# Kernel tuning notes

Hardware: AMD Instinct MI355X
Metric: run time of the kernel (lower is better)

The kernel has to match this reference:

```python
import jax, jax.numpy as jnp
import numpy as np

SHAPES = [(64, 64), (32, 32), (16, 16), (8, 8)]  # (H, W) per level, sum HW = 5440
DIMS, NH, NLVL, NPTS, D_HEIGHT, NCAM, NQ, BS = 256, 8, 4, 8, 4, 6, 10000, 1


def ms_deform_attn(value, shapes, loc, attw):
    # value [B, sumHW, nH, dh]; loc [B, nq, nH, L, P, 2] in [0,1]; attw [B, nq, nH, L, P]
    B, _, nH, dh = value.shape
    nq, P = loc.shape[1], loc.shape[4]
    out = jnp.zeros((B, nH, nq, dh), value.dtype)
    start = 0
    for lvl, (h, w) in enumerate(shapes):
        v = value[:, start:start + h * w].transpose(0, 2, 1, 3)  # [B,nH,hw,dh]
        start += h * w
        l = loc[:, :, :, lvl].transpose(0, 2, 1, 3, 4)  # [B,nH,nq,P,2]
        x = l[..., 0] * w - 0.5
        y = l[..., 1] * h - 0.5
        x0, y0 = jnp.floor(x), jnp.floor(y)
        acc = jnp.zeros((B, nH, nq, P, dh), value.dtype)
        for dy in (0.0, 1.0):
            for dx in (0.0, 1.0):
                cx, cy = x0 + dx, y0 + dy
                wgt = (1.0 - jnp.abs(x - cx)) * (1.0 - jnp.abs(y - cy))
                valid = (cx >= 0) & (cx < w) & (cy >= 0) & (cy < h)
                xi = jnp.clip(cx, 0, w - 1).astype(jnp.int32)
                yi = jnp.clip(cy, 0, h - 1).astype(jnp.int32)
                idx = (yi * w + xi).reshape(B, nH, -1)  # [B,nH,nq*P]
                g = jnp.take_along_axis(v, idx[..., None], axis=2).reshape(B, nH, nq, P, dh)
                acc = acc + jnp.where(valid, wgt, 0.0)[..., None] * g
        aw = attw[:, :, :, lvl].transpose(0, 2, 1, 3)  # [B,nH,nq,P]
        out = out + jnp.einsum('bhqp,bhqpd->bhqd', aw, acc)
    return out.transpose(0, 2, 1, 3).reshape(B, nq, nH * dh)


def setup_inputs() -> dict:
    key = jax.random.key(0)
    ks = jax.random.split(key, 16)
    l = sum(h * w for h, w in SHAPES)
    s = 1.0 / np.sqrt(DIMS)
    inp = {
        'query': jax.random.normal(ks[0], (BS, NQ, DIMS), jnp.float32),
        'key': jax.random.normal(ks[1], (NCAM, l, BS, DIMS), jnp.float32),
        'value': jax.random.normal(ks[2], (NCAM, l, BS, DIMS), jnp.float32),
        'ref_points': jax.random.uniform(ks[3], (NCAM, BS, NQ, D_HEIGHT, 2), jnp.float32),
        'vox_mask': jax.random.randint(ks[4], (NCAM, BS, NQ, D_HEIGHT), 0, 2) > 0,
        'spatial_shapes': np.array(SHAPES, dtype=np.int64),
        'level_start_index': np.array([0, 4096, 5120, 5376], dtype=np.int64),
        'value_W': jax.random.uniform(ks[5], (DIMS, DIMS), jnp.float32, -s, s),
        'value_b': jnp.zeros((DIMS,), jnp.float32),
        'off_W': jax.random.normal(ks[6], (DIMS, NH * NLVL * NPTS * 2), jnp.float32) * 0.01,
        'off_b': jax.random.normal(ks[7], (NH * NLVL * NPTS * 2,), jnp.float32) * 0.1,
        'attw_W': jax.random.normal(ks[8], (DIMS, NH * NLVL * NPTS), jnp.float32) * 0.02,
        'attw_b': jnp.zeros((NH * NLVL * NPTS,), jnp.float32),
        'out_W': jax.random.uniform(ks[9], (DIMS, DIMS), jnp.float32, -s, s),
        'out_b': jnp.zeros((DIMS,), jnp.float32),
    }
    return inp


def reference(query, key, value, ref_points, vox_mask, spatial_shapes, level_start_index,
              value_W, value_b, off_W, off_b, attw_W, attw_b, out_W, out_b):
    shapes = [(int(h), int(w)) for h, w in np.asarray(spatial_shapes)]
    bs, nq, dims = query.shape
    cam = vox_mask.shape[0]
    B = bs * cam
    nH = NH
    dh = dims // nH
    Lv, P, D = len(shapes), NPTS, ref_points.shape[3]

    # value_proj; key unused by deformable attention math
    v = value.transpose(2, 0, 1, 3).reshape(B, -1, dims)
    v = (v @ value_W + value_b).reshape(B, -1, nH, dh)

    # rebatch: every camera sees the full (batch-0 visible) query set; padded
    # entries in the original are discarded, so computing all and masking is exact.
    q = jnp.broadcast_to(query[:, None], (bs, cam, nq, dims)).reshape(B, nq, dims)

    off = (q @ off_W + off_b).reshape(B, nq, nH, Lv, P, 2)
    attw = jax.nn.softmax((q @ attw_W + attw_b).reshape(B, nq, nH, Lv * P), -1)
    attw = attw.reshape(B, nq, nH, Lv, P)

    norm = jnp.array([[w, h] for h, w in shapes], q.dtype)  # [Lv,2] -> (W,H)
    off = off / norm[None, None, None, :, None, :]

    ref_rb = ref_points.transpose(1, 0, 2, 3, 4).reshape(B, nq, D, 2)
    off = off.reshape(B, nq, nH, Lv, P // D, D, 2)
    loc = (ref_rb[:, :, None, None, None] + off).reshape(B, nq, nH, Lv, P, 2)

    out = ms_deform_attn(v, shapes, loc, attw).reshape(bs, cam, nq, dims)

    valid = (vox_mask[:, 0].sum(-1) > 0).astype(q.dtype)  # [cam,nq] (batch-0 indexes, as original)
    slots = jnp.einsum('cq,bcqd->bqd', valid, out)
    count = (vox_mask.sum(-1) > 0).transpose(1, 2, 0).sum(-1).astype(q.dtype)
    count = jnp.maximum(count, 1.0)
    slots = slots / count[..., None]
    slots = slots @ out_W + out_b
    return slots + query  # dropout = identity (eval); inp_residual = query
```

## Files before the change

kernel.cpp:

```cpp
#include <hip/hip_runtime.h>


typedef unsigned short ushort_t;
typedef unsigned int uint_t;
typedef __attribute__((ext_vector_type(8))) short bf16x8;
typedef __attribute__((ext_vector_type(4))) float f32x4;
typedef __attribute__((ext_vector_type(2))) float f32x2;

__device__ __forceinline__ float bf2f(ushort_t u) {
    return __uint_as_float(((uint_t)u) << 16);
}
__device__ __forceinline__ ushort_t f2bf(float f) {
    uint_t i = __float_as_uint(f);
    uint_t r = i + 0x7fffu + ((i >> 16) & 1u);
    return (ushort_t)(r >> 16);
}

__global__ __launch_bounds__(256) void prep_k(
    const float* __restrict__ value, const float* __restrict__ query,
    const float* __restrict__ Wv, const float* __restrict__ Wo,
    const float* __restrict__ Wf, const float* __restrict__ Wa,
    ushort_t* __restrict__ value_bf, ushort_t* __restrict__ query_bf,
    ushort_t* __restrict__ Tv, ushort_t* __restrict__ To,
    ushort_t* __restrict__ Tqk) {
    __shared__ float tile[32][33];
    const int b = blockIdx.x;
    const int tid = threadIdx.x;

    if (b < 5330) {
        const float* src;
        ushort_t* dst;
        int i, n8;
        if (b < 4080) { src = value; dst = value_bf; i = b * 256 + tid;           n8 = 1044480; }
        else          { src = query; dst = query_bf; i = (b - 4080) * 256 + tid;  n8 = 320000; }
        if (i >= n8) return;
        const float4 v0 = *(const float4*)(src + (size_t)i * 8);
        const float4 v1 = *(const float4*)(src + (size_t)i * 8 + 4);
        const bf16x8 pk = {
            (short)f2bf(v0.x), (short)f2bf(v0.y), (short)f2bf(v0.z), (short)f2bf(v0.w),
            (short)f2bf(v1.x), (short)f2bf(v1.y), (short)f2bf(v1.z), (short)f2bf(v1.w)};
        *(bf16x8*)(dst + (size_t)i * 8) = pk;
        return;
    }

    const int b2 = b - 5330;
    const int z   = b2 >> 7;
    const int rem = b2 & 127;
    const int k0 = (rem & 7) * 32;
    const int n0 = (rem >> 3) * 32;
    const float* W;
    ushort_t* T;
    int N;
    if (z == 0)      { W = Wv; T = Tv;              N = 256; }
    else if (z == 1) { W = Wo; T = To;              N = 256; }
    else if (z == 2) { W = Wf; T = Tqk;             N = 512; }
    else             { W = Wa; T = Tqk + 512 * 256; N = 256; }
    if (n0 >= N) return;

    const int tx = tid & 31;
    const int ty = tid >> 5;
    #pragma unroll
    for (int r = 0; r < 4; ++r) {
        const int k = ty + r * 8;
        tile[k][tx] = W[(size_t)(k0 + k) * N + n0 + tx];
    }
    __syncthreads();
    #pragma unroll
    for (int r = 0; r < 4; ++r) {
        const int n = ty + r * 8;
        T[(size_t)(n0 + n) * 256 + k0 + tx] = f2bf(tile[tx][n]);
    }
}

template <bool OUT_BF16, bool RESID>
__global__ __launch_bounds__(256) void gemm_mfma(
    const ushort_t* __restrict__ A, const ushort_t* __restrict__ Wt,
    const float* __restrict__ bias0, const float* __restrict__ bias1, int split,
    const float* __restrict__ resid, void* __restrict__ Cv, int M, int N) {
    __shared__ ushort_t sA[2][128][32];
    __shared__ ushort_t sB[2][128][32];

    const int m0 = blockIdx.x * 128;
    const int n0 = blockIdx.y * 128;
    const int t    = threadIdx.x;
    const int lane = t & 63;
    const int w    = t >> 6;
    const int wr   = w >> 1, wc = w & 1;

    const int srow = t >> 2;
    const int skof = (t & 3) * 8;

    const bool am0 = (m0 + srow) < M;
    const bool am1 = (m0 + 64 + srow) < M;
    const ushort_t* Ap0 = A + (size_t)(m0 + srow) * 256 + skof;
    const ushort_t* Ap1 = Ap0 + (size_t)64 * 256;
    const ushort_t* Bp0 = Wt + (size_t)(n0 + srow) * 256 + skof;
    const ushort_t* Bp1 = Bp0 + (size_t)64 * 256;

    f32x4 acc[4][4];
    #pragma unroll
    for (int i = 0; i < 4; ++i)
        #pragma unroll
        for (int j = 0; j < 4; ++j)
            acc[i][j] = (f32x4){0.f, 0.f, 0.f, 0.f};

    const bf16x8 zz = {0, 0, 0, 0, 0, 0, 0, 0};

    {
        const bf16x8 a0 = am0 ? *(const bf16x8*)(Ap0) : zz;
        const bf16x8 a1 = am1 ? *(const bf16x8*)(Ap1) : zz;
        const bf16x8 b0 = *(const bf16x8*)(Bp0);
        const bf16x8 b1 = *(const bf16x8*)(Bp1);
        *(bf16x8*)(&sA[0][srow][skof])      = a0;
        *(bf16x8*)(&sA[0][64 + srow][skof]) = a1;
        *(bf16x8*)(&sB[0][srow][skof])      = b0;
        *(bf16x8*)(&sB[0][64 + srow][skof]) = b1;
    }
    __syncthreads();

    const int rl = lane & 15;
    const int kq = (lane >> 4) * 8;

    for (int k = 0; k < 8; ++k) {
        const int buf = k & 1;

        bf16x8 na0 = zz, na1 = zz, nb0 = zz, nb1 = zz;
        if (k < 7) {
            const int ko = (k + 1) * 32;
            if (am0) na0 = *(const bf16x8*)(Ap0 + ko);
            if (am1) na1 = *(const bf16x8*)(Ap1 + ko);
            nb0 = *(const bf16x8*)(Bp0 + ko);
            nb1 = *(const bf16x8*)(Bp1 + ko);
        }

        bf16x8 af[4], bfr[4];
        #pragma unroll
        for (int i = 0; i < 4; ++i)
            af[i] = *(const bf16x8*)(&sA[buf][wr * 64 + i * 16 + rl][kq]);
        #pragma unroll
        for (int j = 0; j < 4; ++j)
            bfr[j] = *(const bf16x8*)(&sB[buf][wc * 64 + j * 16 + rl][kq]);
        #pragma unroll
        for (int i = 0; i < 4; ++i)
            #pragma unroll
            for (int j = 0; j < 4; ++j)
                acc[i][j] = __builtin_amdgcn_mfma_f32_16x16x32_bf16(
                    af[i], bfr[j], acc[i][j], 0, 0, 0);

        if (k < 7) {
            __syncthreads();
            *(bf16x8*)(&sA[buf ^ 1][srow][skof])      = na0;
            *(bf16x8*)(&sA[buf ^ 1][64 + srow][skof]) = na1;
            *(bf16x8*)(&sB[buf ^ 1][srow][skof])      = nb0;
            *(bf16x8*)(&sB[buf ^ 1][64 + srow][skof]) = nb1;
            __syncthreads();
        }
    }

    const int col_l = lane & 15;
    const int rq    = (lane >> 4) * 4;
    #pragma unroll
    for (int j = 0; j < 4; ++j) {
        const int gn = n0 + wc * 64 + j * 16 + col_l;
        const float bj = (gn < split) ? bias0[gn] : bias1[gn - split];
        #pragma unroll
        for (int i = 0; i < 4; ++i) {
            #pragma unroll
            for (int r = 0; r < 4; ++r) {
                const int gm = m0 + wr * 64 + i * 16 + rq + r;
                if (gm >= M) continue;
                float v = acc[i][j][r] + bj;
                if (RESID) v += resid[(size_t)gm * N + gn];
                if (OUT_BF16)
                    ((ushort_t*)Cv)[(size_t)gm * N + gn] = f2bf(v);
                else
                    ((float*)Cv)[(size_t)gm * N + gn] = v;
            }
        }
    }
}

__global__ __launch_bounds__(256) void sample_k(
    const float* __restrict__ qkcat,
    const float* __restrict__ refp,
    const int* __restrict__ vox,
    const ushort_t* __restrict__ vproj,
    ushort_t* __restrict__ slots) {
    const int q   = blockIdx.x;
    const int tid = threadIdx.x;
    const int h     = tid >> 5;
    const int lp    = tid & 31;
    const int slice = (tid >> 2) & 7;
    const int g     = tid & 3;

    __shared__ float s_valid[8];
    __shared__ int   s_ci[4][256];
    __shared__ float s_cw[4][256];
    __shared__ float s_red[256][8];

    if (tid < 6) {
        const int base = (tid * 10000 + q) * 4;
        const int mm = vox[base] | vox[base + 1] | vox[base + 2] | vox[base + 3];
        s_valid[tid] = mm ? 1.0f : 0.0f;
    }

    const float a = qkcat[(size_t)q * 768 + 512 + tid];
    float mx = a;
    #pragma unroll
    for (int o = 16; o >= 1; o >>= 1) mx = fmaxf(mx, __shfl_xor(mx, o));
    const float e = __expf(a - mx);
    float se = e;
    #pragma unroll
    for (int o = 16; o >= 1; o >>= 1) se += __shfl_xor(se, o);
    const float aw = e / se;

    const int lvl = lp >> 3;
    const int p   = lp & 7;
    const int dd  = p & 3;
    const int   Sarr[4]   = {64, 32, 16, 8};
    const int   Lstart[4] = {0, 4096, 5120, 5376};
    const int   S  = Sarr[lvl];
    const float Sf = (float)S;
    const int   lstart = Lstart[lvl];
    const float ox = qkcat[(size_t)q * 768 + h * 64 + lvl * 16 + p * 2 + 0] / Sf;
    const float oy = qkcat[(size_t)q * 768 + h * 64 + lvl * 16 + p * 2 + 1] / Sf;

    __syncthreads();
    const float cnt = s_valid[0] + s_valid[1] + s_valid[2] +
                      s_valid[3] + s_valid[4] + s_valid[5];

    f32x2 acc2[4] = {{0.f, 0.f}, {0.f, 0.f}, {0.f, 0.f}, {0.f, 0.f}};
    const ushort_t* vp = vproj + (g << 3);

    for (int c = 0; c < 6; ++c) {
        if (s_valid[c] == 0.0f) continue;

        {
            const int rbase = ((c * 10000 + q) * 4 + dd) * 2;
            const float rx = refp[rbase + 0];
            const float ry = refp[rbase + 1];
            const float x  = (rx + ox) * Sf - 0.5f;
            const float y  = (ry + oy) * Sf - 0.5f;
            const float x0 = floorf(x), y0 = floorf(y);
            #pragma unroll
            for (int k = 0; k < 4; ++k) {
                const float cx = x0 + (float)(k & 1);
                const float cy = y0 + (float)(k >> 1);
                const float wgt = (1.0f - fabsf(x - cx)) * (1.0f - fabsf(y - cy));
                const bool ok = (cx >= 0.0f) & (cx < Sf) & (cy >= 0.0f) & (cy < Sf);
                const int xi = (int)fminf(fmaxf(cx, 0.0f), Sf - 1.0f);
                const int yi = (int)fminf(fmaxf(cy, 0.0f), Sf - 1.0f);
                s_ci[k][tid] = (c * 5440 + lstart + yi * S + xi) * 256 + h * 32;
                s_cw[k][tid] = ok ? wgt * aw : 0.0f;
            }
        }
        __syncthreads();

        #pragma unroll
        for (int j = 0; j < 4; ++j) {
            const int el = h * 32 + slice * 4 + j;
            const int i0 = s_ci[0][el], i1 = s_ci[1][el];
            const int i2 = s_ci[2][el], i3 = s_ci[3][el];
            const float w0 = s_cw[0][el], w1 = s_cw[1][el];
            const float w2 = s_cw[2][el], w3 = s_cw[3][el];
            const uint4 v0 = *(const uint4*)(vp + i0);
            const uint4 v1 = *(const uint4*)(vp + i1);
            const uint4 v2 = *(const uint4*)(vp + i2);
            const uint4 v3 = *(const uint4*)(vp + i3);
            const f32x2 W0 = {w0, w0}, W1 = {w1, w1}, W2 = {w2, w2}, W3 = {w3, w3};
            acc2[0] += W0 * (f32x2){__uint_as_float(v0.x << 16),
                                    __uint_as_float(v0.x & 0xffff0000u)};
            acc2[1] += W0 * (f32x2){__uint_as_float(v0.y << 16),
                                    __uint_as_float(v0.y & 0xffff0000u)};
            acc2[2] += W0 * (f32x2){__uint_as_float(v0.z << 16),
                                    __uint_as_float(v0.z & 0xffff0000u)};
            acc2[3] += W0 * (f32x2){__uint_as_float(v0.w << 16),
                                    __uint_as_float(v0.w & 0xffff0000u)};
            acc2[0] += W1 * (f32x2){__uint_as_float(v1.x << 16),
                                    __uint_as_float(v1.x & 0xffff0000u)};
            acc2[1] += W1 * (f32x2){__uint_as_float(v1.y << 16),
                                    __uint_as_float(v1.y & 0xffff0000u)};
            acc2[2] += W1 * (f32x2){__uint_as_float(v1.z << 16),
                                    __uint_as_float(v1.z & 0xffff0000u)};
            acc2[3] += W1 * (f32x2){__uint_as_float(v1.w << 16),
                                    __uint_as_float(v1.w & 0xffff0000u)};
            acc2[0] += W2 * (f32x2){__uint_as_float(v2.x << 16),
                                    __uint_as_float(v2.x & 0xffff0000u)};
            acc2[1] += W2 * (f32x2){__uint_as_float(v2.y << 16),
                                    __uint_as_float(v2.y & 0xffff0000u)};
            acc2[2] += W2 * (f32x2){__uint_as_float(v2.z << 16),
                                    __uint_as_float(v2.z & 0xffff0000u)};
            acc2[3] += W2 * (f32x2){__uint_as_float(v2.w << 16),
                                    __uint_as_float(v2.w & 0xffff0000u)};
            acc2[0] += W3 * (f32x2){__uint_as_float(v3.x << 16),
                                    __uint_as_float(v3.x & 0xffff0000u)};
            acc2[1] += W3 * (f32x2){__uint_as_float(v3.y << 16),
                                    __uint_as_float(v3.y & 0xffff0000u)};
            acc2[2] += W3 * (f32x2){__uint_as_float(v3.z << 16),
                                    __uint_as_float(v3.z & 0xffff0000u)};
            acc2[3] += W3 * (f32x2){__uint_as_float(v3.w << 16),
                                    __uint_as_float(v3.w & 0xffff0000u)};
        }
        __syncthreads();
    }

    #pragma unroll
    for (int n = 0; n < 4; ++n) {
        s_red[tid][2 * n]     = acc2[n].x;
        s_red[tid][2 * n + 1] = acc2[n].y;
    }
    __syncthreads();

    const int cch = tid & 31;
    float sum = 0.0f;
    #pragma unroll
    for (int s = 0; s < 8; ++s)
        sum += s_red[h * 32 + s * 4 + (cch >> 3)][cch & 7];

    slots[(size_t)q * 256 + tid] = f2bf(sum / fmaxf(cnt, 1.0f));
}

extern "C" void kernel_launch(void* const* d_in, const int* in_sizes, int n_in,
                              void* d_out, int out_size, void* d_ws, size_t ws_size,
                              hipStream_t stream) {
    const float* query   = (const float*)d_in[0];
    const float* value   = (const float*)d_in[2];
    const float* refp    = (const float*)d_in[3];
    const int*   vox     = (const int*)d_in[4];
    const float* value_W = (const float*)d_in[7];
    const float* value_b = (const float*)d_in[8];
    const float* off_W   = (const float*)d_in[9];
    const float* off_b   = (const float*)d_in[10];
    const float* attw_W  = (const float*)d_in[11];
    const float* attw_b  = (const float*)d_in[12];
    const float* out_W   = (const float*)d_in[13];
    const float* out_b   = (const float*)d_in[14];
    float* out = (float*)d_out;

    char* ws = (char*)d_ws;
    ushort_t* vproj    = (ushort_t*)ws;
    ushort_t* value_bf = (ushort_t*)(ws + 16711680);
    float*    qkcat    = (float*)   (ws + 16711680);
    ushort_t* query_bf = (ushort_t*)(ws + 47431680);
    ushort_t* slots    = (ushort_t*)(ws + 47431680);
    ushort_t* value_Wt = (ushort_t*)(ws + 52551680);
    ushort_t* out_Wt   = (ushort_t*)(ws + 52551680 + 131072);
    ushort_t* qk_Wt    = (ushort_t*)(ws + 52551680 + 262144);

    prep_k<<<5842, 256, 0, stream>>>(value, query, value_W, out_W, off_W, attw_W,
                                     value_bf, query_bf, value_Wt, out_Wt, qk_Wt);
    gemm_mfma<true, false><<<dim3(255, 2), 256, 0, stream>>>(
        value_bf, value_Wt, value_b, value_b, 256, nullptr,
        (void*)vproj, 32640, 256);
    gemm_mfma<false, false><<<dim3(79, 6), 256, 0, stream>>>(
        query_bf, qk_Wt, off_b, attw_b, 512, nullptr,
        (void*)qkcat, 10000, 768);
    sample_k<<<10000, 256, 0, stream>>>(qkcat, refp, vox, vproj, slots);
    gemm_mfma<false, true><<<dim3(79, 2), 256, 0, stream>>>(
        slots, out_Wt, out_b, out_b, 256, query, (void*)out, 10000, 256);
}
```

Measured before the change: 337.8 us.

## Fuse all stages into one persistent cooperative kernel with grid syncs

Replaces the five separate launches (prep, two projection GEMMs, sampling, output GEMM) with a single persistent cooperative kernel. Blocks loop over work units and are separated by grid-wide barriers, with a shared-memory union reused across stages. It also shrinks the GEMM tiles to 64x64 and stores the offset/attention projection in bf16 instead of fp32, halving that buffer's traffic. The intent is to remove launch gaps and tail effects. In exchange it adds grid-sync cost, gives smaller GEMM tiles less reuse, caps the grid at 1024 blocks, and lowers the precision of the sampling offsets and attention logits.

```diff
diff --git a/kernel.cpp b/kernel.cpp
--- a/kernel.cpp
+++ b/kernel.cpp
@@ -1,4 +1,5 @@
 #include <hip/hip_runtime.h>
+#include <hip/hip_cooperative_groups.h>
 
 
 typedef unsigned short ushort_t;
@@ -16,23 +17,31 @@
     return (ushort_t)(r >> 16);
 }
 
-__global__ __launch_bounds__(256) void prep_k(
+struct GemmSmem  { ushort_t sA[2][64][32]; ushort_t sB[2][64][32]; };
+struct SampleSmem {
+    float valid[8];
+    int   ci[4][256];
+    float cw[4][256];
+    float red[256][8];
+};
+struct PrepSmem  { float tile[32][33]; };
+union SmemAll { GemmSmem g; SampleSmem s; PrepSmem p; };
+
+__device__ __forceinline__ void prep_unit(
+    int u, PrepSmem* sp,
     const float* __restrict__ value, const float* __restrict__ query,
     const float* __restrict__ Wv, const float* __restrict__ Wo,
     const float* __restrict__ Wf, const float* __restrict__ Wa,
     ushort_t* __restrict__ value_bf, ushort_t* __restrict__ query_bf,
     ushort_t* __restrict__ Tv, ushort_t* __restrict__ To,
     ushort_t* __restrict__ Tqk) {
-    __shared__ float tile[32][33];
-    const int b = blockIdx.x;
     const int tid = threadIdx.x;
-
-    if (b < 5330) {
+    if (u < 5330) {
         const float* src;
         ushort_t* dst;
         int i, n8;
-        if (b < 4080) { src = value; dst = value_bf; i = b * 256 + tid;           n8 = 1044480; }
-        else          { src = query; dst = query_bf; i = (b - 4080) * 256 + tid;  n8 = 320000; }
+        if (u < 4080) { src = value; dst = value_bf; i = u * 256 + tid;          n8 = 1044480; }
+        else          { src = query; dst = query_bf; i = (u - 4080) * 256 + tid; n8 = 320000; }
         if (i >= n8) return;
         const float4 v0 = *(const float4*)(src + (size_t)i * 8);
         const float4 v1 = *(const float4*)(src + (size_t)i * 8 + 4);
@@ -42,8 +51,7 @@
         *(bf16x8*)(dst + (size_t)i * 8) = pk;
         return;
     }
-
-    const int b2 = b - 5330;
+    const int b2 = u - 5330;
     const int z   = b2 >> 7;
     const int rem = b2 & 127;
     const int k0 = (rem & 7) * 32;
@@ -62,149 +70,109 @@
     #pragma unroll
     for (int r = 0; r < 4; ++r) {
         const int k = ty + r * 8;
-        tile[k][tx] = W[(size_t)(k0 + k) * N + n0 + tx];
+        sp->tile[k][tx] = W[(size_t)(k0 + k) * N + n0 + tx];
     }
     __syncthreads();
     #pragma unroll
     for (int r = 0; r < 4; ++r) {
         const int n = ty + r * 8;
-        T[(size_t)(n0 + n) * 256 + k0 + tx] = f2bf(tile[tx][n]);
-    }
+        T[(size_t)(n0 + n) * 256 + k0 + tx] = f2bf(sp->tile[tx][n]);
+    }
+    __syncthreads();
 }
 
 template <bool OUT_BF16, bool RESID>
-__global__ __launch_bounds__(256) void gemm_mfma(
+__device__ __forceinline__ void gemm64_tile(
+    GemmSmem* sm,
     const ushort_t* __restrict__ A, const ushort_t* __restrict__ Wt,
     const float* __restrict__ bias0, const float* __restrict__ bias1, int split,
-    const float* __restrict__ resid, void* __restrict__ Cv, int M, int N) {
-    __shared__ ushort_t sA[2][128][32];
-    __shared__ ushort_t sB[2][128][32];
-
-    const int m0 = blockIdx.x * 128;
-    const int n0 = blockIdx.y * 128;
-    const int t    = threadIdx.x;
-    const int lane = t & 63;
-    const int w    = t >> 6;
-    const int wr   = w >> 1, wc = w & 1;
-
+    const float* __restrict__ resid, void* __restrict__ Cv,
+    int M, int N, int u) {
+    const int tn = N >> 6;
+    const int bx = u / tn;
+    const int by = u - bx * tn;
+    const int m0 = bx << 6, n0 = by << 6;
+    const int t = threadIdx.x, lane = t & 63, w = t >> 6;
     const int srow = t >> 2;
-    const int skof = (t & 3) * 8;
-
-    const bool am0 = (m0 + srow) < M;
-    const bool am1 = (m0 + 64 + srow) < M;
-    const ushort_t* Ap0 = A + (size_t)(m0 + srow) * 256 + skof;
-    const ushort_t* Ap1 = Ap0 + (size_t)64 * 256;
-    const ushort_t* Bp0 = Wt + (size_t)(n0 + srow) * 256 + skof;
-    const ushort_t* Bp1 = Bp0 + (size_t)64 * 256;
-
-    f32x4 acc[4][4];
-    #pragma unroll
-    for (int i = 0; i < 4; ++i)
+    const int skof = (t & 3) << 3;
+    const bool am = (m0 + srow) < M;
+    const ushort_t* Ap = A + (size_t)(m0 + srow) * 256 + skof;
+    const ushort_t* Bp = Wt + (size_t)(n0 + srow) * 256 + skof;
+    const bf16x8 zz = {0, 0, 0, 0, 0, 0, 0, 0};
+
+    f32x4 acc[4];
+    #pragma unroll
+    for (int j = 0; j < 4; ++j) acc[j] = (f32x4){0.f, 0.f, 0.f, 0.f};
+
+    *(bf16x8*)(&sm->sA[0][srow][skof]) = am ? *(const bf16x8*)Ap : zz;
+    *(bf16x8*)(&sm->sB[0][srow][skof]) = *(const bf16x8*)Bp;
+    __syncthreads();
+
+    const int rl = lane & 15;
+    const int kq = (lane >> 4) << 3;
+
+    for (int k = 0; k < 8; ++k) {
+        const int buf = k & 1;
+        bf16x8 na = zz, nb = zz;
+        if (k < 7) {
+            const int ko = (k + 1) << 5;
+            if (am) na = *(const bf16x8*)(Ap + ko);
+            nb = *(const bf16x8*)(Bp + ko);
+        }
+        const bf16x8 af = *(const bf16x8*)(&sm->sA[buf][(w << 4) + rl][kq]);
+        bf16x8 bfr[4];
         #pragma unroll
         for (int j = 0; j < 4; ++j)
-            acc[i][j] = (f32x4){0.f, 0.f, 0.f, 0.f};
-
-    const bf16x8 zz = {0, 0, 0, 0, 0, 0, 0, 0};
-
-    {
-        const bf16x8 a0 = am0 ? *(const bf16x8*)(Ap0) : zz;
-        const bf16x8 a1 = am1 ? *(const bf16x8*)(Ap1) : zz;
-        const bf16x8 b0 = *(const bf16x8*)(Bp0);
-        const bf16x8 b1 = *(const bf16x8*)(Bp1);
-        *(bf16x8*)(&sA[0][srow][skof])      = a0;
-        *(bf16x8*)(&sA[0][64 + srow][skof]) = a1;
-        *(bf16x8*)(&sB[0][srow][skof])      = b0;
-        *(bf16x8*)(&sB[0][64 + srow][skof]) = b1;
-    }
-    __syncthreads();
-
-    const int rl = lane & 15;
-    const int kq = (lane >> 4) * 8;
-
-    for (int k = 0; k < 8; ++k) {
-        const int buf = k & 1;
-
-        bf16x8 na0 = zz, na1 = zz, nb0 = zz, nb1 = zz;
-        if (k < 7) {
-            const int ko = (k + 1) * 32;
-            if (am0) na0 = *(const bf16x8*)(Ap0 + ko);
-            if (am1) na1 = *(const bf16x8*)(Ap1 + ko);
-            nb0 = *(const bf16x8*)(Bp0 + ko);
-            nb1 = *(const bf16x8*)(Bp1 + ko);
-        }
-
-        bf16x8 af[4], bfr[4];
-        #pragma unroll
-        for (int i = 0; i < 4; ++i)
-            af[i] = *(const bf16x8*)(&sA[buf][wr * 64 + i * 16 + rl][kq]);
+            bfr[j] = *(const bf16x8*)(&sm->sB[buf][(j << 4) + rl][kq]);
         #pragma unroll
         for (int j = 0; j < 4; ++j)
-            bfr[j] = *(const bf16x8*)(&sB[buf][wc * 64 + j * 16 + rl][kq]);
-        #pragma unroll
-        for (int i = 0; i < 4; ++i)
-            #pragma unroll
-            for (int j = 0; j < 4; ++j)
-                acc[i][j] = __builtin_amdgcn_mfma_f32_16x16x32_bf16(
-                    af[i], bfr[j], acc[i][j], 0, 0, 0);
-
+            acc[j] = __builtin_amdgcn_mfma_f32_16x16x32_bf16(af, bfr[j], acc[j], 0, 0, 0);
         if (k < 7) {
             __syncthreads();
-            *(bf16x8*)(&sA[buf ^ 1][srow][skof])      = na0;
-            *(bf16x8*)(&sA[buf ^ 1][64 + srow][skof]) = na1;
-            *(bf16x8*)(&sB[buf ^ 1][srow][skof])      = nb0;
-            *(bf16x8*)(&sB[buf ^ 1][64 + srow][skof]) = nb1;
+            *(bf16x8*)(&sm->sA[buf ^ 1][srow][skof]) = na;
+            *(bf16x8*)(&sm->sB[buf ^ 1][srow][skof]) = nb;
             __syncthreads();
         }
     }
 
     const int col_l = lane & 15;
-    const int rq    = (lane >> 4) * 4;
+    const int rq = (lane >> 4) << 2;
     #pragma unroll
     for (int j = 0; j < 4; ++j) {
-        const int gn = n0 + wc * 64 + j * 16 + col_l;
+        const int gn = n0 + (j << 4) + col_l;
         const float bj = (gn < split) ? bias0[gn] : bias1[gn - split];
         #pragma unroll
-        for (int i = 0; i < 4; ++i) {
-            #pragma unroll
-            for (int r = 0; r < 4; ++r) {
-                const int gm = m0 + wr * 64 + i * 16 + rq + r;
-                if (gm >= M) continue;
-                float v = acc[i][j][r] + bj;
-                if (RESID) v += resid[(size_t)gm * N + gn];
-                if (OUT_BF16)
-                    ((ushort_t*)Cv)[(size_t)gm * N + gn] = f2bf(v);
-                else
-                    ((float*)Cv)[(size_t)gm * N + gn] = v;
-            }
-        }
-    }
-}
-
-__global__ __launch_bounds__(256) void sample_k(
-    const float* __restrict__ qkcat,
-    const float* __restrict__ refp,
-    const int* __restrict__ vox,
-    const ushort_t* __restrict__ vproj,
+        for (int r = 0; r < 4; ++r) {
+            const int gm = m0 + (w << 4) + rq + r;
+            if (gm >= M) continue;
+            float v = acc[j][r] + bj;
+            if (RESID) v += resid[(size_t)gm * N + gn];
+            if (OUT_BF16)
+                ((ushort_t*)Cv)[(size_t)gm * N + gn] = f2bf(v);
+            else
+                ((float*)Cv)[(size_t)gm * N + gn] = v;
+        }
+    }
+}
+
+__device__ __forceinline__ void sample_unit(
+    int q, SampleSmem* ss,
+    const ushort_t* __restrict__ qkcat, const float* __restrict__ refp,
+    const int* __restrict__ vox, const ushort_t* __restrict__ vproj,
     ushort_t* __restrict__ slots) {
-    const int q   = blockIdx.x;
     const int tid = threadIdx.x;
     const int h     = tid >> 5;
     const int lp    = tid & 31;
     const int slice = (tid >> 2) & 7;
     const int g     = tid & 3;
 
-    __shared__ float s_valid[8];
-    __shared__ int   s_ci[4][256];
-    __shared__ float s_cw[4][256];
-    __shared__ float s_red[256][8];
-
     if (tid < 6) {
         const int base = (tid * 10000 + q) * 4;
         const int mm = vox[base] | vox[base + 1] | vox[base + 2] | vox[base + 3];
-        s_valid[tid] = mm ? 1.0f : 0.0f;
-    }
-
-    const float a = qkcat[(size_t)q * 768 + 512 + tid];
+        ss->valid[tid] = mm ? 1.0f : 0.0f;
+    }
+
+    const float a = bf2f(qkcat[(size_t)q * 768 + 512 + tid]);
     float mx = a;
     #pragma unroll
     for (int o = 16; o >= 1; o >>= 1) mx = fmaxf(mx, __shfl_xor(mx, o));
@@ -221,19 +189,20 @@
     const int   Lstart[4] = {0, 4096, 5120, 5376};
     const int   S  = Sarr[lvl];
     const float Sf = (float)S;
+    const float invSf = 1.0f / Sf;
     const int   lstart = Lstart[lvl];
-    const float ox = qkcat[(size_t)q * 768 + h * 64 + lvl * 16 + p * 2 + 0] / Sf;
-    const float oy = qkcat[(size_t)q * 768 + h * 64 + lvl * 16 + p * 2 + 1] / Sf;
-
-    __syncthreads();
-    const float cnt = s_valid[0] + s_valid[1] + s_valid[2] +
-                      s_valid[3] + s_valid[4] + s_valid[5];
+    const float ox = bf2f(qkcat[(size_t)q * 768 + h * 64 + lvl * 16 + p * 2 + 0]) * invSf;
+    const float oy = bf2f(qkcat[(size_t)q * 768 + h * 64 + lvl * 16 + p * 2 + 1]) * invSf;
+
+    __syncthreads();
+    const float cnt = ss->valid[0] + ss->valid[1] + ss->valid[2] +
+                      ss->valid[3] + ss->valid[4] + ss->valid[5];
 
     f32x2 acc2[4] = {{0.f, 0.f}, {0.f, 0.f}, {0.f, 0.f}, {0.f, 0.f}};
     const ushort_t* vp = vproj + (g << 3);
 
     for (int c = 0; c < 6; ++c) {
-        if (s_valid[c] == 0.0f) continue;
+        if (ss->valid[c] == 0.0f) continue;
 
         {
             const int rbase = ((c * 10000 + q) * 4 + dd) * 2;
@@ -250,8 +219,8 @@
                 const bool ok = (cx >= 0.0f) & (cx < Sf) & (cy >= 0.0f) & (cy < Sf);
                 const int xi = (int)fminf(fmaxf(cx, 0.0f), Sf - 1.0f);
                 const int yi = (int)fminf(fmaxf(cy, 0.0f), Sf - 1.0f);
-                s_ci[k][tid] = (c * 5440 + lstart + yi * S + xi) * 256 + h * 32;
-                s_cw[k][tid] = ok ? wgt * aw : 0.0f;
+                ss->ci[k][tid] = (c * 5440 + lstart + yi * S + xi) * 256 + h * 32;
+                ss->cw[k][tid] = ok ? wgt * aw : 0.0f;
             }
         }
         __syncthreads();
@@ -259,55 +228,39 @@
         #pragma unroll
         for (int j = 0; j < 4; ++j) {
             const int el = h * 32 + slice * 4 + j;
-            const int i0 = s_ci[0][el], i1 = s_ci[1][el];
-            const int i2 = s_ci[2][el], i3 = s_ci[3][el];
-            const float w0 = s_cw[0][el], w1 = s_cw[1][el];
-            const float w2 = s_cw[2][el], w3 = s_cw[3][el];
+            const int i0 = ss->ci[0][el], i1 = ss->ci[1][el];
+            const int i2 = ss->ci[2][el], i3 = ss->ci[3][el];
+            const float w0 = ss->cw[0][el], w1 = ss->cw[1][el];
+            const float w2 = ss->cw[2][el], w3 = ss->cw[3][el];
             const uint4 v0 = *(const uint4*)(vp + i0);
             const uint4 v1 = *(const uint4*)(vp + i1);
             const uint4 v2 = *(const uint4*)(vp + i2);
             const uint4 v3 = *(const uint4*)(vp + i3);
             const f32x2 W0 = {w0, w0}, W1 = {w1, w1}, W2 = {w2, w2}, W3 = {w3, w3};
-            acc2[0] += W0 * (f32x2){__uint_as_float(v0.x << 16),
-                                    __uint_as_float(v0.x & 0xffff0000u)};
-            acc2[1] += W0 * (f32x2){__uint_as_float(v0.y << 16),
-                                    __uint_as_float(v0.y & 0xffff0000u)};
-            acc2[2] += W0 * (f32x2){__uint_as_float(v0.z << 16),
-                                    __uint_as_float(v0.z & 0xffff0000u)};
-            acc2[3] += W0 * (f32x2){__uint_as_float(v0.w << 16),
-                                    __uint_as_float(v0.w & 0xffff0000u)};
-            acc2[0] += W1 * (f32x2){__uint_as_float(v1.x << 16),
-                                    __uint_as_float(v1.x & 0xffff0000u)};
-            acc2[1] += W1 * (f32x2){__uint_as_float(v1.y << 16),
-                                    __uint_as_float(v1.y & 0xffff0000u)};
-            acc2[2] += W1 * (f32x2){__uint_as_float(v1.z << 16),
-                                    __uint_as_float(v1.z & 0xffff0000u)};
-            acc2[3] += W1 * (f32x2){__uint_as_float(v1.w << 16),
-                                    __uint_as_float(v1.w & 0xffff0000u)};
-            acc2[0] += W2 * (f32x2){__uint_as_float(v2.x << 16),
-                                    __uint_as_float(v2.x & 0xffff0000u)};
-            acc2[1] += W2 * (f32x2){__uint_as_float(v2.y << 16),
-                                    __uint_as_float(v2.y & 0xffff0000u)};
-            acc2[2] += W2 * (f32x2){__uint_as_float(v2.z << 16),
-                                    __uint_as_float(v2.z & 0xffff0000u)};
-            acc2[3] += W2 * (f32x2){__uint_as_float(v2.w << 16),
-                                    __uint_as_float(v2.w & 0xffff0000u)};
-            acc2[0] += W3 * (f32x2){__uint_as_float(v3.x << 16),
-                                    __uint_as_float(v3.x & 0xffff0000u)};
-            acc2[1] += W3 * (f32x2){__uint_as_float(v3.y << 16),
-                                    __uint_as_float(v3.y & 0xffff0000u)};
-            acc2[2] += W3 * (f32x2){__uint_as_float(v3.z << 16),
-                                    __uint_as_float(v3.z & 0xffff0000u)};
-            acc2[3] += W3 * (f32x2){__uint_as_float(v3.w << 16),
-                                    __uint_as_float(v3.w & 0xffff0000u)};
+            acc2[0] += W0 * (f32x2){__uint_as_float(v0.x << 16), __uint_as_float(v0.x & 0xffff0000u)};
+            acc2[1] += W0 * (f32x2){__uint_as_float(v0.y << 16), __uint_as_float(v0.y & 0xffff0000u)};
+            acc2[2] += W0 * (f32x2){__uint_as_float(v0.z << 16), __uint_as_float(v0.z & 0xffff0000u)};
+            acc2[3] += W0 * (f32x2){__uint_as_float(v0.w << 16), __uint_as_float(v0.w & 0xffff0000u)};
+            acc2[0] += W1 * (f32x2){__uint_as_float(v1.x << 16), __uint_as_float(v1.x & 0xffff0000u)};
+            acc2[1] += W1 * (f32x2){__uint_as_float(v1.y << 16), __uint_as_float(v1.y & 0xffff0000u)};
+            acc2[2] += W1 * (f32x2){__uint_as_float(v1.z << 16), __uint_as_float(v1.z & 0xffff0000u)};
+            acc2[3] += W1 * (f32x2){__uint_as_float(v1.w << 16), __uint_as_float(v1.w & 0xffff0000u)};
+            acc2[0] += W2 * (f32x2){__uint_as_float(v2.x << 16), __uint_as_float(v2.x & 0xffff0000u)};
+            acc2[1] += W2 * (f32x2){__uint_as_float(v2.y << 16), __uint_as_float(v2.y & 0xffff0000u)};
+            acc2[2] += W2 * (f32x2){__uint_as_float(v2.z << 16), __uint_as_float(v2.z & 0xffff0000u)};
+            acc2[3] += W2 * (f32x2){__uint_as_float(v2.w << 16), __uint_as_float(v2.w & 0xffff0000u)};
+            acc2[0] += W3 * (f32x2){__uint_as_float(v3.x << 16), __uint_as_float(v3.x & 0xffff0000u)};
+            acc2[1] += W3 * (f32x2){__uint_as_float(v3.y << 16), __uint_as_float(v3.y & 0xffff0000u)};
+            acc2[2] += W3 * (f32x2){__uint_as_float(v3.z << 16), __uint_as_float(v3.z & 0xffff0000u)};
+            acc2[3] += W3 * (f32x2){__uint_as_float(v3.w << 16), __uint_as_float(v3.w & 0xffff0000u)};
         }
         __syncthreads();
     }
 
     #pragma unroll
     for (int n = 0; n < 4; ++n) {
-        s_red[tid][2 * n]     = acc2[n].x;
-        s_red[tid][2 * n + 1] = acc2[n].y;
+        ss->red[tid][2 * n]     = acc2[n].x;
+        ss->red[tid][2 * n + 1] = acc2[n].y;
     }
     __syncthreads();
 
@@ -315,9 +268,50 @@
     float sum = 0.0f;
     #pragma unroll
     for (int s = 0; s < 8; ++s)
-        sum += s_red[h * 32 + s * 4 + (cch >> 3)][cch & 7];
+        sum += ss->red[h * 32 + s * 4 + (cch >> 3)][cch & 7];
 
     slots[(size_t)q * 256 + tid] = f2bf(sum / fmaxf(cnt, 1.0f));
+}
+
+__global__ __launch_bounds__(256, 4) void fused_k(
+    const float* __restrict__ query, const float* __restrict__ value,
+    const float* __restrict__ refp, const int* __restrict__ vox,
+    const float* __restrict__ value_W, const float* __restrict__ value_b,
+    const float* __restrict__ off_W, const float* __restrict__ off_b,
+    const float* __restrict__ attw_W, const float* __restrict__ attw_b,
+    const float* __restrict__ out_W, const float* __restrict__ out_b,
+    float* __restrict__ out,
+    ushort_t* __restrict__ value_bf, ushort_t* __restrict__ query_bf,
+    ushort_t* __restrict__ vproj, ushort_t* __restrict__ qkcat,
+    ushort_t* __restrict__ slots,
+    ushort_t* __restrict__ value_Wt, ushort_t* __restrict__ out_Wt,
+    ushort_t* __restrict__ qk_Wt) {
+    cooperative_groups::grid_group grid = cooperative_groups::this_grid();
+    __shared__ SmemAll sm;
+    const int nb = gridDim.x;
+
+    for (int u = blockIdx.x; u < 5842; u += nb)
+        prep_unit(u, &sm.p, value, query, value_W, out_W, off_W, attw_W,
+                  value_bf, query_bf, value_Wt, out_Wt, qk_Wt);
+    grid.sync();
+
+    for (int u = blockIdx.x; u < 3924; u += nb) {
+        if (u < 2040)
+            gemm64_tile<true, false>(&sm.g, value_bf, value_Wt, value_b, value_b,
+                                     256, nullptr, (void*)vproj, 32640, 256, u);
+        else
+            gemm64_tile<true, false>(&sm.g, query_bf, qk_Wt, off_b, attw_b,
+                                     512, nullptr, (void*)qkcat, 10000, 768, u - 2040);
+    }
+    grid.sync();
+
+    for (int q = blockIdx.x; q < 10000; q += nb)
+        sample_unit(q, &sm.s, qkcat, refp, vox, vproj, slots);
+    grid.sync();
+
+    for (int u = blockIdx.x; u < 628; u += nb)
+        gemm64_tile<false, true>(&sm.g, slots, out_Wt, out_b, out_b, 256,
+                                 query, (void*)out, 10000, 256, u);
 }
 
 extern "C" void kernel_launch(void* const* d_in, const int* in_sizes, int n_in,
@@ -338,24 +332,28 @@
     float* out = (float*)d_out;
 
     char* ws = (char*)d_ws;
-    ushort_t* vproj    = (ushort_t*)ws;
+    ushort_t* vproj    = (ushort_t*)(ws);
     ushort_t* value_bf = (ushort_t*)(ws + 16711680);
-    float*    qkcat    = (float*)   (ws + 16711680);
-    ushort_t* query_bf = (ushort_t*)(ws + 47431680);
-    ushort_t* slots    = (ushort_t*)(ws + 47431680);
-    ushort_t* value_Wt = (ushort_t*)(ws + 52551680);
-    ushort_t* out_Wt   = (ushort_t*)(ws + 52551680 + 131072);
-    ushort_t* qk_Wt    = (ushort_t*)(ws + 52551680 + 262144);
-
-    prep_k<<<5842, 256, 0, stream>>>(value, query, value_W, out_W, off_W, attw_W,
-                                     value_bf, query_bf, value_Wt, out_Wt, qk_Wt);
-    gemm_mfma<true, false><<<dim3(255, 2), 256, 0, stream>>>(
-        value_bf, value_Wt, value_b, value_b, 256, nullptr,
-        (void*)vproj, 32640, 256);
-    gemm_mfma<false, false><<<dim3(79, 6), 256, 0, stream>>>(
-        query_bf, qk_Wt, off_b, attw_b, 512, nullptr,
-        (void*)qkcat, 10000, 768);
-    sample_k<<<10000, 256, 0, stream>>>(qkcat, refp, vox, vproj, slots);
-    gemm_mfma<false, true><<<dim3(79, 2), 256, 0, stream>>>(
-        slots, out_Wt, out_b, out_b, 256, query, (void*)out, 10000, 256);
-}
+    ushort_t* slots    = (ushort_t*)(ws + 16711680);
+    ushort_t* qkcat    = (ushort_t*)(ws + 33423360);
+    ushort_t* query_bf = (ushort_t*)(ws + 48783360);
+    ushort_t* value_Wt = (ushort_t*)(ws + 53903360);
+    ushort_t* out_Wt   = (ushort_t*)(ws + 53903360 + 131072);
+    ushort_t* qk_Wt    = (ushort_t*)(ws + 53903360 + 262144);
+
+    int maxB = 0;
+    hipError_t oe = hipOccupancyMaxActiveBlocksPerMultiprocessor(&maxB, fused_k, 256, 0);
+    if (oe != hipSuccess || maxB < 1) maxB = 1;
+    unsigned nblk = (unsigned)maxB * 256u;
+    if (nblk > 1024u) nblk = 1024u;
+
+    void* args[] = {
+        (void*)&query, (void*)&value, (void*)&refp, (void*)&vox,
+        (void*)&value_W, (void*)&value_b, (void*)&off_W, (void*)&off_b,
+        (void*)&attw_W, (void*)&attw_b, (void*)&out_W, (void*)&out_b,
+        (void*)&out,
+        (void*)&value_bf, (void*)&query_bf, (void*)&vproj, (void*)&qkcat,
+        (void*)&slots, (void*)&value_Wt, (void*)&out_Wt, (void*)&qk_Wt};
+    hipLaunchCooperativeKernel((void*)fused_k, dim3(nblk), dim3(256),
+                               args, 0, stream);
+}
```

After: 759.9 us. 125% more time.
